# Kernel optimization log

Measured on AMD Instinct MI355X. Metric: run time of the kernel, lower is better.

## Reference

```python
import jax, jax.numpy as jnp
import numpy as np

DN = ('NCHW', 'OIHW', 'NCHW')

def conv2d(x, w, pad):
    return jax.lax.conv_general_dilated(x, w, (1, 1), [(pad, pad), (pad, pad)], dimension_numbers=DN)

def conv_module(x, w, g, b):
    # Conv2d -> BN (inference-mode per-channel affine) -> ReLU
    pad = (w.shape[-1] - 1) // 2
    y = conv2d(x, w, pad)
    return jax.nn.relu(y * g[None, :, None, None] + b[None, :, None, None])

def seq_conv_module(x, w, g, b):
    # x: (T, B, C, H, W) -> apply ConvModule per frame by folding T into batch
    T, B, C, H, W = x.shape
    y = conv_module(x.reshape(T * B, C, H, W), w, g, b)
    return y.reshape(T, B, -1, H, W)

def setup_inputs() -> dict:
    key = jax.random.key(0)
    ks = jax.random.split(key, 32)
    Cin, Ck, Cv, Cout = 1024, 256, 512, 512
    T, B, H, W = 4, 1, 64, 64
    s = 0.02
    d = {}
    d['x'] = jax.random.normal(ks[0], (B, Cin, H, W), jnp.float32)
    d['seq'] = jax.random.normal(ks[1], (T, B, Cin, H, W), jnp.float32)
    def mk_cm(i, cin, cout, k):
        return (jax.random.normal(ks[i], (cout, cin, k, k), jnp.float32) * s,
                jnp.ones((cout,), jnp.float32),
                jnp.zeros((cout,), jnp.float32))
    d['wk1'], d['gk1'], d['bk1'] = mk_cm(2, Cin, Ck, 1)
    d['wk2'], d['gk2'], d['bk2'] = mk_cm(3, Ck, Ck, 3)
    d['wv1'], d['gv1'], d['bv1'] = mk_cm(4, Cin, Cv, 1)
    d['wv2'], d['gv2'], d['bv2'] = mk_cm(5, Cv, Cv, 3)
    d['wqk1'], d['gqk1'], d['bqk1'] = mk_cm(6, Cin, Ck, 1)
    d['wqk2'], d['gqk2'], d['bqk2'] = mk_cm(7, Ck, Ck, 3)
    d['wqv1'], d['gqv1'], d['bqv1'] = mk_cm(8, Cin, Cv, 1)
    d['wqv2'], d['gqv2'], d['bqv2'] = mk_cm(9, Cv, Cv, 3)
    d['wb'], d['gb'], d['bb'] = mk_cm(10, 2 * Cv, Cout, 3)
    return d

def reference(x, seq, wk1, gk1, bk1, wk2, gk2, bk2, wv1, gv1, bv1, wv2, gv2, bv2,
              wqk1, gqk1, bqk1, wqk2, gqk2, bqk2, wqv1, gqv1, bqv1, wqv2, gqv2, bqv2,
              wb, gb, bb):
    # memory key/value convs over the T reference frames
    mk = seq_conv_module(seq_conv_module(seq, wk1, gk1, bk1), wk2, gk2, bk2)  # (T,B,Ck,H,W)
    mv = seq_conv_module(seq_conv_module(seq, wv1, gv1, bv1), wv2, gv2, bv2)  # (T,B,Cv,H,W)
    # query key/value convs on current frame
    qk = conv_module(conv_module(x, wqk1, gqk1, bqk1), wqk2, gqk2, bqk2)      # (B,Ck,H,W)
    qv = conv_module(conv_module(x, wqv1, gqv1, bqv1), wqv2, gqv2, bqv2)      # (B,Cv,H,W)
    T, B, Ck, H, W = mk.shape
    Cv = mv.shape[2]
    mk = jnp.transpose(mk, (1, 2, 0, 3, 4)).reshape(B, Ck, T * H * W)         # (B,Ck,THW)
    mv = jnp.transpose(mv, (1, 2, 0, 3, 4)).reshape(B, Cv, T * H * W)         # (B,Cv,THW)
    qkf = qk.reshape(B, Ck, H * W)                                            # (B,Ck,HW)
    # attention: (B,HW,THW); matmul_norm=False so no 1/sqrt(Ck) scaling
    attn = jax.nn.softmax(jnp.einsum('bcq,bck->bqk', qkf, mk), axis=-1)
    mem = jnp.einsum('bqk,bck->bcq', attn, mv).reshape(B, Cv, H, W)
    out = conv_module(jnp.concatenate([qv, mem], axis=1), wb, gb, bb)
    return out
```

## Files before the change

kernel.cpp:

```cpp
#include <hip/hip_runtime.h>
#include <stdint.h>


typedef short bf16x8 __attribute__((ext_vector_type(8)));
typedef float f32x4  __attribute__((ext_vector_type(4)));
typedef unsigned short u16x4 __attribute__((ext_vector_type(4)));

__device__ __forceinline__ unsigned short f2bf(float f) {
  union { float f; unsigned u; } x; x.f = f;
  unsigned r = x.u + 0x7FFFu + ((x.u >> 16) & 1u);
  return (unsigned short)(r >> 16);
}

typedef const __attribute__((address_space(1))) char* as1cp;
typedef __attribute__((address_space(3))) char* as3p;

__device__ __forceinline__ void gl_lds16(const char* g, char* l) {
  __builtin_amdgcn_global_load_lds((as1cp)g, (as3p)l, 16, 0, 0);
}

enum { EP_CL_BNR = 0, EP_CF_BNR_BF16 = 1, EP_CF_BNR_F32 = 2, EP_EXPSUM = 3,
       EP_PVDIV = 4, EP_PART = 5 };

template<int EP, bool CF, bool CONV3>
__global__ __launch_bounds__(256) void gemm_k(
    const unsigned short* __restrict__ Wp,
    const unsigned short* __restrict__ Xp,
    int K, int Kc, int Xstride, int Xcoloff, int cin_log2,
    void* __restrict__ Op, int Ostride, int Ocoloff, size_t plane,
    const float* __restrict__ g1, const float* __restrict__ b1,
    const float* __restrict__ g2, const float* __restrict__ b2, int gsplit,
    float* __restrict__ rowsum, const char* __restrict__ zp)
{
  __shared__ short Wt[2][128 * 32];
  __shared__ short Xt[2][128 * 32];
  const int tid = threadIdx.x;
  const int w = tid >> 6;
  const int l = tid & 63;
  const int m0 = blockIdx.y * 128;
  const int n0 = blockIdx.x * 128;
  const int wrow0 = CF ? n0 : m0;
  const int xrow0 = CF ? m0 : n0;

  const int ch0 = w, ch1 = w + 4;
  const int sr0 = ch0 * 16 + (l >> 2);
  const int sr1 = ch1 * 16 + (l >> 2);
  const int kbp = (l & 3) << 4;
  const int kbl0 = kbp ^ ((sr0 & 3) << 4);
  const int kbl1 = kbp ^ ((sr1 & 3) << 4);

  const size_t wrb = (size_t)K * 2;
  const size_t xrb = (size_t)Xstride * 2;

  const int wm = (w >> 1) * 64;
  const int wn = (w & 1) * 64;

  const int k_begin = blockIdx.z * Kc;
  const int k_end = (k_begin + Kc < K) ? (k_begin + Kc) : K;

  auto stage = [&](int b, int k0) {
    int ci0 = k0, kh = 1, kw = 1, dpos = 0;
    if (CONV3) {
      int e = k0 >> cin_log2;
      ci0 = k0 & ((1 << cin_log2) - 1);
      kh = e / 3; kw = e - kh * 3;
      dpos = (kh - 1) * 64 + (kw - 1);
    }
    char* Wl = (char*)&Wt[b][0];
    char* Xl = (char*)&Xt[b][0];
    gl_lds16((const char*)Wp + (size_t)(wrow0 + sr0) * wrb + (size_t)k0 * 2 + kbl0,
             Wl + ch0 * 1024);
    gl_lds16((const char*)Wp + (size_t)(wrow0 + sr1) * wrb + (size_t)k0 * 2 + kbl1,
             Wl + ch1 * 1024);
    const char* xs0;
    const char* xs1;
    if (CONV3) {
      int p = xrow0 + sr0;
      int hw = p & 4095;
      int h2 = (hw >> 6) + kh - 1, w2 = (hw & 63) + kw - 1;
      xs0 = ((unsigned)h2 < 64u && (unsigned)w2 < 64u)
          ? (const char*)Xp + (size_t)(p + dpos) * xrb + (size_t)(Xcoloff + ci0) * 2 + kbl0
          : zp + kbl0;
      p = xrow0 + sr1;
      hw = p & 4095;
      h2 = (hw >> 6) + kh - 1; w2 = (hw & 63) + kw - 1;
      xs1 = ((unsigned)h2 < 64u && (unsigned)w2 < 64u)
          ? (const char*)Xp + (size_t)(p + dpos) * xrb + (size_t)(Xcoloff + ci0) * 2 + kbl1
          : zp + kbl1;
    } else {
      xs0 = (const char*)Xp + (size_t)(xrow0 + sr0) * xrb + (size_t)(Xcoloff + k0) * 2 + kbl0;
      xs1 = (const char*)Xp + (size_t)(xrow0 + sr1) * xrb + (size_t)(Xcoloff + k0) * 2 + kbl1;
    }
    gl_lds16(xs0, Xl + ch0 * 1024);
    gl_lds16(xs1, Xl + ch1 * 1024);
  };

  f32x4 acc[4][4] = {};

  int cur = 0;
  stage(0, k_begin);
  for (int k0 = k_begin; k0 < k_end; k0 += 32) {
    if (k0 + 32 < k_end) {
      stage(cur ^ 1, k0 + 32);
      asm volatile("s_waitcnt vmcnt(4)" ::: "memory");
    } else {
      asm volatile("s_waitcnt vmcnt(0)" ::: "memory");
    }
    __builtin_amdgcn_s_barrier();

    const short* Wb = &Wt[cur][0];
    const short* Xb = &Xt[cur][0];
    const short* At = CF ? Xb : Wb;
    const short* Bt = CF ? Wb : Xb;

    bf16x8 af[4], bfv[4];
#pragma unroll
    for (int i = 0; i < 4; i++) {
      int row = wm + i * 16 + (l & 15);
      int kb = ((l >> 4) << 4) ^ ((row & 3) << 4);
      af[i] = *(const bf16x8*)(At + row * 32 + (kb >> 1));
    }
#pragma unroll
    for (int j = 0; j < 4; j++) {
      int row = wn + j * 16 + (l & 15);
      int kb = ((l >> 4) << 4) ^ ((row & 3) << 4);
      bfv[j] = *(const bf16x8*)(Bt + row * 32 + (kb >> 1));
    }
#pragma unroll
    for (int i = 0; i < 4; i++)
#pragma unroll
      for (int j = 0; j < 4; j++)
        acc[i][j] = __builtin_amdgcn_mfma_f32_16x16x32_bf16(af[i], bfv[j], acc[i][j], 0, 0, 0);

    __builtin_amdgcn_s_barrier();
    cur ^= 1;
  }

  const int col = l & 15;
  const int rb = (l >> 4) << 2;

  if constexpr (EP == EP_PART) {
    float* P = (float*)Op + (size_t)blockIdx.z * plane;
#pragma unroll
    for (int j = 0; j < 4; j++) {
      int gn = n0 + wn + j * 16 + col;
#pragma unroll
      for (int i = 0; i < 4; i++) {
        int gm = m0 + wm + i * 16 + rb;
        *(f32x4*)(P + (size_t)gn * Ostride + gm) = acc[i][j];
      }
    }
  }
  if constexpr (EP == EP_CL_BNR) {
#pragma unroll
    for (int i = 0; i < 4; i++) {
      int gm = m0 + wm + i * 16 + rb;
      const float* gp; const float* bp;
      if (gm < gsplit) { gp = g1 + gm; bp = b1 + gm; }
      else             { gp = g2 + (gm - gsplit); bp = b2 + (gm - gsplit); }
      float G[4], B[4];
#pragma unroll
      for (int r = 0; r < 4; r++) { G[r] = gp[r]; B[r] = bp[r]; }
#pragma unroll
      for (int j = 0; j < 4; j++) {
        int gn = n0 + wn + j * 16 + col;
        f32x4 v = acc[i][j];
        u16x4 o;
#pragma unroll
        for (int r = 0; r < 4; r++) o[r] = f2bf(fmaxf(v[r] * G[r] + B[r], 0.f));
        *(u16x4*)((unsigned short*)Op + (size_t)gn * Ostride + Ocoloff + gm) = o;
      }
    }
  }
  if constexpr (EP == EP_CF_BNR_BF16 || EP == EP_CF_BNR_F32) {
#pragma unroll
    for (int j = 0; j < 4; j++) {
      int gn = n0 + wn + j * 16 + col;
      float G = (gn < gsplit) ? g1[gn] : g2[gn - gsplit];
      float Bv = (gn < gsplit) ? b1[gn] : b2[gn - gsplit];
#pragma unroll
      for (int i = 0; i < 4; i++) {
        int gm = m0 + wm + i * 16 + rb;
        f32x4 v = acc[i][j];
        if constexpr (EP == EP_CF_BNR_F32) {
          f32x4 o;
#pragma unroll
          for (int r = 0; r < 4; r++) o[r] = fmaxf(v[r] * G + Bv, 0.f);
          *(f32x4*)((float*)Op + (size_t)gn * Ostride + Ocoloff + gm) = o;
        } else {
          u16x4 o;
#pragma unroll
          for (int r = 0; r < 4; r++) o[r] = f2bf(fmaxf(v[r] * G + Bv, 0.f));
          *(u16x4*)((unsigned short*)Op + (size_t)gn * Ostride + Ocoloff + gm) = o;
        }
      }
    }
  }
  if constexpr (EP == EP_EXPSUM) {
#pragma unroll
    for (int j = 0; j < 4; j++) {
      int gn = n0 + wn + j * 16 + col;
      float s = 0.f;
#pragma unroll
      for (int i = 0; i < 4; i++) {
        int gm = m0 + wm + i * 16 + rb;
        f32x4 v = acc[i][j];
        u16x4 o;
#pragma unroll
        for (int r = 0; r < 4; r++) { float e = __expf(v[r]); s += e; o[r] = f2bf(e); }
        *(u16x4*)((unsigned short*)Op + (size_t)gn * Ostride + gm) = o;
      }
      s += __shfl_xor(s, 16);
      s += __shfl_xor(s, 32);
      if (l < 16) atomicAdd(rowsum + gn, s);
    }
  }
  if constexpr (EP == EP_PVDIV) {
#pragma unroll
    for (int j = 0; j < 4; j++) {
      int gn = n0 + wn + j * 16 + col;
      float inv = 1.0f / rowsum[gn];
#pragma unroll
      for (int i = 0; i < 4; i++) {
        int gm = m0 + wm + i * 16 + rb;
        f32x4 v = acc[i][j];
        u16x4 o;
#pragma unroll
        for (int r = 0; r < 4; r++) o[r] = f2bf(v[r] * inv);
        *(u16x4*)((unsigned short*)Op + (size_t)gn * Ostride + Ocoloff + gm) = o;
      }
    }
  }
}

enum { RED_BNR_BF16 = 0, RED_PVDIV = 1, RED_BNR_F32 = 2 };

template<int MODE>
__global__ __launch_bounds__(256) void reduce_k(
    const float* __restrict__ P, int Z, size_t plane, int Cdim,
    void* __restrict__ out, int Ostride, int Ocoloff,
    const float* __restrict__ g1, const float* __restrict__ b1,
    const float* __restrict__ g2, const float* __restrict__ b2, int gsplit,
    const float* __restrict__ rowsum, int total4)
{
  int t = blockIdx.x * 256 + threadIdx.x;
  if (t >= total4) return;
  size_t base = (size_t)t * 4;
  int n = (int)(base / (size_t)Cdim);
  int c = (int)(base % (size_t)Cdim);
  f32x4 s = *(const f32x4*)(P + base);
  for (int z = 1; z < Z; z++) {
    f32x4 v = *(const f32x4*)(P + (size_t)z * plane + base);
    s += v;
  }
  if constexpr (MODE == RED_BNR_BF16) {
    u16x4 o;
#pragma unroll
    for (int r = 0; r < 4; r++) {
      int ch = c + r;
      float G = (ch < gsplit) ? g1[ch] : g2[ch - gsplit];
      float B = (ch < gsplit) ? b1[ch] : b2[ch - gsplit];
      o[r] = f2bf(fmaxf(s[r] * G + B, 0.f));
    }
    *(u16x4*)((unsigned short*)out + (size_t)n * Ostride + Ocoloff + c) = o;
  }
  if constexpr (MODE == RED_PVDIV) {
    float inv = 1.0f / rowsum[n];
    u16x4 o;
#pragma unroll
    for (int r = 0; r < 4; r++) o[r] = f2bf(s[r] * inv);
    *(u16x4*)((unsigned short*)out + (size_t)n * Ostride + Ocoloff + c) = o;
  }
  if constexpr (MODE == RED_BNR_F32) {
    float G = g1[n], B = b1[n];
    f32x4 o;
#pragma unroll
    for (int r = 0; r < 4; r++) o[r] = fmaxf(s[r] * G + B, 0.f);
    *(f32x4*)((float*)out + (size_t)n * Ostride + c) = o;
  }
}

__global__ __launch_bounds__(256) void nchw_to_cl(const float* __restrict__ src,
                                                  unsigned short* __restrict__ dst,
                                                  int C, int P) {
  __shared__ float t[32][33];
  int f = blockIdx.z;
  src += (size_t)f * C * P;
  dst += (size_t)f * C * P;
  int p0 = blockIdx.x * 32, c0 = blockIdx.y * 32;
  int a = threadIdx.x & 31, b = threadIdx.x >> 5;
#pragma unroll
  for (int k = 0; k < 4; k++)
    t[b + 8 * k][a] = src[(size_t)(c0 + b + 8 * k) * P + p0 + a];
  __syncthreads();
#pragma unroll
  for (int k = 0; k < 4; k++)
    dst[(size_t)(p0 + b + 8 * k) * C + c0 + a] = f2bf(t[a][b + 8 * k]);
}

__global__ __launch_bounds__(256) void cvt_bf16(const float* __restrict__ s,
                                                unsigned short* __restrict__ d, int n) {
  int i = blockIdx.x * 256 + threadIdx.x;
  if (i < n) d[i] = f2bf(s[i]);
}

__global__ __launch_bounds__(256) void repack3(const float* __restrict__ s,
                                               unsigned short* __restrict__ d,
                                               int ci_log2, int n) {
  int i = blockIdx.x * 256 + threadIdx.x;
  if (i >= n) return;
  int Ci = 1 << ci_log2;
  int ci = i & (Ci - 1);
  int t = i >> ci_log2;
  int e = t % 9;
  int co = t / 9;
  d[i] = f2bf(s[((size_t)co * Ci + ci) * 9 + e]);
}

__global__ __launch_bounds__(256) void fillf(float* p, float v, int n) {
  int i = blockIdx.x * 256 + threadIdx.x;
  if (i < n) p[i] = v;
}

extern "C" void kernel_launch(void* const* d_in, const int* in_sizes, int n_in,
                              void* d_out, int out_size, void* d_ws, size_t ws_size,
                              hipStream_t stream) {
  (void)in_sizes; (void)n_in;
  const float* x    = (const float*)d_in[0];
  const float* seq  = (const float*)d_in[1];
  const float* wk1  = (const float*)d_in[2];
  const float* gk1  = (const float*)d_in[3];
  const float* bk1  = (const float*)d_in[4];
  const float* wk2  = (const float*)d_in[5];
  const float* gk2  = (const float*)d_in[6];
  const float* bk2  = (const float*)d_in[7];
  const float* wv1  = (const float*)d_in[8];
  const float* gv1  = (const float*)d_in[9];
  const float* bv1  = (const float*)d_in[10];
  const float* wv2  = (const float*)d_in[11];
  const float* gv2  = (const float*)d_in[12];
  const float* bv2  = (const float*)d_in[13];
  const float* wqk1 = (const float*)d_in[14];
  const float* gqk1 = (const float*)d_in[15];
  const float* bqk1 = (const float*)d_in[16];
  const float* wqk2 = (const float*)d_in[17];
  const float* gqk2 = (const float*)d_in[18];
  const float* bqk2 = (const float*)d_in[19];
  const float* wqv1 = (const float*)d_in[20];
  const float* gqv1 = (const float*)d_in[21];
  const float* bqv1 = (const float*)d_in[22];
  const float* wqv2 = (const float*)d_in[23];
  const float* gqv2 = (const float*)d_in[24];
  const float* bqv2 = (const float*)d_in[25];
  const float* wb   = (const float*)d_in[26];
  const float* gb   = (const float*)d_in[27];
  const float* bb   = (const float*)d_in[28];

  char* ws = (char*)d_ws;
  size_t off = 0;
  auto alloc = [&](size_t bytes) { size_t o = off; off += (bytes + 255) & ~(size_t)255; return o; };
  size_t o_zp    = alloc(4096);
  size_t o_rs    = alloc(4096 * 4);
  size_t o_wKV1  = alloc((size_t)768 * 1024 * 2);
  size_t o_wQKV1 = alloc((size_t)768 * 1024 * 2);
  size_t o_wK2   = alloc((size_t)256 * 2304 * 2);
  size_t o_wQK2  = alloc((size_t)256 * 2304 * 2);
  size_t o_wV2   = alloc((size_t)512 * 4608 * 2);
  size_t o_wQV2  = alloc((size_t)512 * 4608 * 2);
  size_t o_wB    = alloc((size_t)512 * 9216 * 2);
  size_t o_mk    = alloc((size_t)16384 * 256 * 2);
  size_t o_mv    = alloc((size_t)512 * 16384 * 2);
  size_t o_qk    = alloc((size_t)4096 * 256 * 2);
  size_t o_qvm   = alloc((size_t)4096 * 1024 * 2);
  size_t o_part  = alloc((size_t)8 * 4096 * 512 * 4);
  size_t o_vol   = off;
  size_t o_xT    = o_vol;
  size_t o_seqT  = o_xT + (size_t)4096 * 1024 * 2;
  size_t o_kv1   = o_seqT + (size_t)4 * 4096 * 1024 * 2;
  size_t o_qkv1  = o_kv1 + (size_t)16384 * 768 * 2;
  size_t end1    = o_qkv1 + (size_t)4096 * 768 * 2;
  size_t o_expS  = o_vol;
  size_t end2    = o_expS + (size_t)4096 * 16384 * 2;
  size_t need    = end1 > end2 ? end1 : end2;

  bool SPLIT = ws_size >= need;
  if (!SPLIT) {
    size_t save = o_part;
    o_vol  = save;
    o_xT   = o_vol;
    o_seqT = o_xT + (size_t)4096 * 1024 * 2;
    o_kv1  = o_seqT + (size_t)4 * 4096 * 1024 * 2;
    o_qkv1 = o_kv1 + (size_t)16384 * 768 * 2;
    end1   = o_qkv1 + (size_t)4096 * 768 * 2;
    o_expS = o_vol;
    end2   = o_expS + (size_t)4096 * 16384 * 2;
    need   = end1 > end2 ? end1 : end2;
    if (ws_size < need) {
      fillf<<<(out_size + 255) / 256, 256, 0, stream>>>((float*)d_out, 12345.0f, out_size);
      return;
    }
  }

  const char* zp = ws + o_zp;
  float* rs = (float*)(ws + o_rs);
  unsigned short* wKV1p  = (unsigned short*)(ws + o_wKV1);
  unsigned short* wQKV1p = (unsigned short*)(ws + o_wQKV1);
  unsigned short* wK2p   = (unsigned short*)(ws + o_wK2);
  unsigned short* wQK2p  = (unsigned short*)(ws + o_wQK2);
  unsigned short* wV2p   = (unsigned short*)(ws + o_wV2);
  unsigned short* wQV2p  = (unsigned short*)(ws + o_wQV2);
  unsigned short* wBp    = (unsigned short*)(ws + o_wB);
  unsigned short* mkp    = (unsigned short*)(ws + o_mk);
  unsigned short* mvp    = (unsigned short*)(ws + o_mv);
  unsigned short* qkp    = (unsigned short*)(ws + o_qk);
  unsigned short* qvmp   = (unsigned short*)(ws + o_qvm);
  float* partp           = (float*)(ws + o_part);
  unsigned short* xTp    = (unsigned short*)(ws + o_xT);
  unsigned short* seqTp  = (unsigned short*)(ws + o_seqT);
  unsigned short* kv1p   = (unsigned short*)(ws + o_kv1);
  unsigned short* qkv1p  = (unsigned short*)(ws + o_qkv1);
  unsigned short* expSp  = (unsigned short*)(ws + o_expS);

  hipMemsetAsync(ws + o_zp, 0, 4096, stream);
  hipMemsetAsync(ws + o_rs, 0, 4096 * 4, stream);

  cvt_bf16<<<(256 * 1024 + 255) / 256, 256, 0, stream>>>(wk1, wKV1p, 256 * 1024);
  cvt_bf16<<<(512 * 1024 + 255) / 256, 256, 0, stream>>>(wv1, wKV1p + 256 * 1024, 512 * 1024);
  cvt_bf16<<<(256 * 1024 + 255) / 256, 256, 0, stream>>>(wqk1, wQKV1p, 256 * 1024);
  cvt_bf16<<<(512 * 1024 + 255) / 256, 256, 0, stream>>>(wqv1, wQKV1p + 256 * 1024, 512 * 1024);
  repack3<<<(256 * 2304 + 255) / 256, 256, 0, stream>>>(wk2, wK2p, 8, 256 * 2304);
  repack3<<<(256 * 2304 + 255) / 256, 256, 0, stream>>>(wqk2, wQK2p, 8, 256 * 2304);
  repack3<<<(512 * 4608 + 255) / 256, 256, 0, stream>>>(wv2, wV2p, 9, 512 * 4608);
  repack3<<<(512 * 4608 + 255) / 256, 256, 0, stream>>>(wqv2, wQV2p, 9, 512 * 4608);
  repack3<<<(512 * 9216 + 255) / 256, 256, 0, stream>>>(wb, wBp, 10, 512 * 9216);

  nchw_to_cl<<<dim3(128, 32, 1), 256, 0, stream>>>(x, xTp, 1024, 4096);
  nchw_to_cl<<<dim3(128, 32, 4), 256, 0, stream>>>(seq, seqTp, 1024, 4096);

  gemm_k<EP_CL_BNR, false, false><<<dim3(128, 6), 256, 0, stream>>>(
      wKV1p, seqTp, 1024, 1024, 1024, 0, 0, kv1p, 768, 0, 0,
      gk1, bk1, gv1, bv1, 256, rs, zp);
  if (SPLIT) {
    size_t plane = (size_t)4096 * 768;
    gemm_k<EP_PART, false, false><<<dim3(32, 6, 2), 256, 0, stream>>>(
        wQKV1p, xTp, 1024, 512, 1024, 0, 0, partp, 768, 0, plane,
        nullptr, nullptr, nullptr, nullptr, 0, rs, zp);
    int t4 = (int)(plane / 4);
    reduce_k<RED_BNR_BF16><<<(t4 + 255) / 256, 256, 0, stream>>>(
        partp, 2, plane, 768, qkv1p, 768, 0, gqk1, bqk1, gqv1, bqv1, 256, rs, t4);
  } else {
    gemm_k<EP_CL_BNR, false, false><<<dim3(32, 6), 256, 0, stream>>>(
        wQKV1p, xTp, 1024, 1024, 1024, 0, 0, qkv1p, 768, 0, 0,
        gqk1, bqk1, gqv1, bqv1, 256, rs, zp);
  }

  gemm_k<EP_CL_BNR, false, true><<<dim3(128, 2), 256, 0, stream>>>(
      wK2p, kv1p, 2304, 2304, 768, 0, 8, mkp, 256, 0, 0,
      gk2, bk2, gk2, bk2, 256, rs, zp);
  if (SPLIT) {
    size_t plane = (size_t)4096 * 256;
    gemm_k<EP_PART, false, true><<<dim3(32, 2, 4), 256, 0, stream>>>(
        wQK2p, qkv1p, 2304, 576, 768, 0, 8, partp, 256, 0, plane,
        nullptr, nullptr, nullptr, nullptr, 0, rs, zp);
    int t4 = (int)(plane / 4);
    reduce_k<RED_BNR_BF16><<<(t4 + 255) / 256, 256, 0, stream>>>(
        partp, 4, plane, 256, qkp, 256, 0, gqk2, bqk2, gqk2, bqk2, 256, rs, t4);
  } else {
    gemm_k<EP_CL_BNR, false, true><<<dim3(32, 2), 256, 0, stream>>>(
        wQK2p, qkv1p, 2304, 2304, 768, 0, 8, qkp, 256, 0, 0,
        gqk2, bqk2, gqk2, bqk2, 256, rs, zp);
  }
  if (SPLIT) {
    size_t plane = (size_t)4096 * 512;
    gemm_k<EP_PART, false, true><<<dim3(32, 4, 4), 256, 0, stream>>>(
        wQV2p, qkv1p, 4608, 1152, 768, 256, 9, partp, 512, 0, plane,
        nullptr, nullptr, nullptr, nullptr, 0, rs, zp);
    int t4 = (int)(plane / 4);
    reduce_k<RED_BNR_BF16><<<(t4 + 255) / 256, 256, 0, stream>>>(
        partp, 4, plane, 512, qvmp, 1024, 0, gqv2, bqv2, gqv2, bqv2, 512, rs, t4);
  } else {
    gemm_k<EP_CL_BNR, false, true><<<dim3(32, 4), 256, 0, stream>>>(
        wQV2p, qkv1p, 4608, 4608, 768, 256, 9, qvmp, 1024, 0, 0,
        gqv2, bqv2, gqv2, bqv2, 512, rs, zp);
  }
  gemm_k<EP_CF_BNR_BF16, true, true><<<dim3(4, 128), 256, 0, stream>>>(
      wV2p, kv1p, 4608, 4608, 768, 256, 9, mvp, 16384, 0, 0,
      gv2, bv2, gv2, bv2, 512, rs, zp);

  gemm_k<EP_EXPSUM, false, false><<<dim3(32, 128), 256, 0, stream>>>(
      mkp, qkp, 256, 256, 256, 0, 0, expSp, 16384, 0, 0,
      nullptr, nullptr, nullptr, nullptr, 1 << 30, rs, zp);
  if (SPLIT) {
    size_t plane = (size_t)4096 * 512;
    gemm_k<EP_PART, false, false><<<dim3(32, 4, 8), 256, 0, stream>>>(
        mvp, expSp, 16384, 2048, 16384, 0, 0, partp, 512, 0, plane,
        nullptr, nullptr, nullptr, nullptr, 0, rs, zp);
    int t4 = (int)(plane / 4);
    reduce_k<RED_PVDIV><<<(t4 + 255) / 256, 256, 0, stream>>>(
        partp, 8, plane, 512, qvmp, 1024, 512, nullptr, nullptr, nullptr, nullptr, 0, rs, t4);
  } else {
    gemm_k<EP_PVDIV, false, false><<<dim3(32, 4), 256, 0, stream>>>(
        mvp, expSp, 16384, 16384, 16384, 0, 0, qvmp, 1024, 512, 0,
        nullptr, nullptr, nullptr, nullptr, 1 << 30, rs, zp);
  }

  if (SPLIT) {
    size_t plane = (size_t)512 * 4096;
    gemm_k<EP_PART, true, true><<<dim3(4, 32, 4), 256, 0, stream>>>(
        wBp, qvmp, 9216, 2304, 1024, 0, 10, partp, 4096, 0, plane,
        nullptr, nullptr, nullptr, nullptr, 0, rs, zp);
    int t4 = (int)(plane / 4);
    reduce_k<RED_BNR_F32><<<(t4 + 255) / 256, 256, 0, stream>>>(
        partp, 4, plane, 4096, (float*)d_out, 4096, 0, gb, bb, gb, bb, 512, rs, t4);
  } else {
    gemm_k<EP_CF_BNR_F32, true, true><<<dim3(4, 32), 256, 0, stream>>>(
        wBp, qvmp, 9216, 9216, 1024, 0, 10, (float*)d_out, 4096, 0, 0,
        gb, bb, gb, bb, 512, rs, zp);
  }
}
```

Baseline: 646.3 us.

## Triple-buffer GEMM LDS pipeline and add wide-tile PV GEMM with blocked exp layout

Measured after the change: 627.3 us. -2.9%, faster.

```diff
diff --git a/kernel.cpp b/kernel.cpp
--- a/kernel.cpp
+++ b/kernel.cpp
@@ -32,8 +32,8 @@
     const float* __restrict__ g2, const float* __restrict__ b2, int gsplit,
     float* __restrict__ rowsum, const char* __restrict__ zp)
 {
-  __shared__ short Wt[2][128 * 32];
-  __shared__ short Xt[2][128 * 32];
+  __shared__ short Wt[3][128 * 32];
+  __shared__ short Xt[3][128 * 32];
   const int tid = threadIdx.x;
   const int w = tid >> 6;
   const int l = tid & 63;
@@ -57,6 +57,7 @@
 
   const int k_begin = blockIdx.z * Kc;
   const int k_end = (k_begin + Kc < K) ? (k_begin + Kc) : K;
+  const int niter = (k_end - k_begin) >> 5;
 
   auto stage = [&](int b, int k0) {
     int ci0 = k0, kh = 1, kw = 1, dpos = 0;
@@ -97,15 +98,16 @@
 
   f32x4 acc[4][4] = {};
 
+  {
+    int nst = niter < 3 ? niter : 3;
+    for (int s = 0; s < nst; ++s) stage(s, k_begin + (s << 5));
+  }
   int cur = 0;
-  stage(0, k_begin);
-  for (int k0 = k_begin; k0 < k_end; k0 += 32) {
-    if (k0 + 32 < k_end) {
-      stage(cur ^ 1, k0 + 32);
-      asm volatile("s_waitcnt vmcnt(4)" ::: "memory");
-    } else {
-      asm volatile("s_waitcnt vmcnt(0)" ::: "memory");
-    }
+  for (int i = 0; i < niter; ++i) {
+    int ahead = niter - i - 1;
+    if (ahead >= 2)      asm volatile("s_waitcnt vmcnt(8)" ::: "memory");
+    else if (ahead == 1) asm volatile("s_waitcnt vmcnt(4)" ::: "memory");
+    else                 asm volatile("s_waitcnt vmcnt(0)" ::: "memory");
     __builtin_amdgcn_s_barrier();
 
     const short* Wb = &Wt[cur][0];
@@ -115,10 +117,10 @@
 
     bf16x8 af[4], bfv[4];
 #pragma unroll
-    for (int i = 0; i < 4; i++) {
-      int row = wm + i * 16 + (l & 15);
+    for (int ii = 0; ii < 4; ii++) {
+      int row = wm + ii * 16 + (l & 15);
       int kb = ((l >> 4) << 4) ^ ((row & 3) << 4);
-      af[i] = *(const bf16x8*)(At + row * 32 + (kb >> 1));
+      af[ii] = *(const bf16x8*)(At + row * 32 + (kb >> 1));
     }
 #pragma unroll
     for (int j = 0; j < 4; j++) {
@@ -127,13 +129,14 @@
       bfv[j] = *(const bf16x8*)(Bt + row * 32 + (kb >> 1));
     }
 #pragma unroll
-    for (int i = 0; i < 4; i++)
+    for (int ii = 0; ii < 4; ii++)
 #pragma unroll
       for (int j = 0; j < 4; j++)
-        acc[i][j] = __builtin_amdgcn_mfma_f32_16x16x32_bf16(af[i], bfv[j], acc[i][j], 0, 0, 0);
+        acc[ii][j] = __builtin_amdgcn_mfma_f32_16x16x32_bf16(af[ii], bfv[j], acc[ii][j], 0, 0, 0);
 
     __builtin_amdgcn_s_barrier();
-    cur ^= 1;
+    if (i + 3 < niter) stage(cur, k_begin + ((i + 3) << 5));
+    cur = cur == 2 ? 0 : cur + 1;
   }
 
   const int col = l & 15;
@@ -208,7 +211,11 @@
         u16x4 o;
 #pragma unroll
         for (int r = 0; r < 4; r++) { float e = __expf(v[r]); s += e; o[r] = f2bf(e); }
-        *(u16x4*)((unsigned short*)Op + (size_t)gn * Ostride + gm) = o;
+        if (gsplit)
+          *(u16x4*)((unsigned short*)Op + (size_t)(gm >> 5) * ((size_t)Ostride * 32)
+                    + (size_t)gn * 32 + (gm & 31)) = o;
+        else
+          *(u16x4*)((unsigned short*)Op + (size_t)gn * Ostride + gm) = o;
       }
       s += __shfl_xor(s, 16);
       s += __shfl_xor(s, 32);
@@ -229,6 +236,98 @@
         for (int r = 0; r < 4; r++) o[r] = f2bf(v[r] * inv);
         *(u16x4*)((unsigned short*)Op + (size_t)gn * Ostride + Ocoloff + gm) = o;
       }
+    }
+  }
+}
+
+__global__ __launch_bounds__(512, 2) void pv_gemm(
+    const unsigned short* __restrict__ Wp,
+    const unsigned short* __restrict__ Xp,
+    int K, int Kc, int qtot,
+    float* __restrict__ P, size_t plane)
+{
+  __shared__ short Wt[3][512 * 32];
+  __shared__ short Xt[3][128 * 32];
+  const int tid = threadIdx.x;
+  const int w = tid >> 6;
+  const int l = tid & 63;
+  const int n0 = blockIdx.x * 128;
+  const int z = blockIdx.y;
+  const int k_begin = z * Kc;
+  const int niter = Kc >> 5;
+  const int kbp = (l & 3) << 4;
+  const size_t wrb = (size_t)K * 2;
+
+  auto stage = [&](int b, int k0) {
+    char* Wl = (char*)&Wt[b][0];
+    char* Xl = (char*)&Xt[b][0];
+#pragma unroll
+    for (int t = 0; t < 4; ++t) {
+      int sr = w * 64 + t * 16 + (l >> 2);
+      int c = kbp ^ ((sr & 3) << 4);
+      gl_lds16((const char*)Wp + (size_t)sr * wrb + (size_t)k0 * 2 + c,
+               Wl + (w * 4 + t) * 1024);
+    }
+    int sx = w * 16 + (l >> 2);
+    int cx = kbp ^ ((sx & 3) << 4);
+    gl_lds16((const char*)Xp + (size_t)(k0 >> 5) * ((size_t)qtot * 64)
+             + (size_t)(n0 + sx) * 64 + cx,
+             Xl + w * 1024);
+  };
+
+  const int wm = (w >> 1) * 128;
+  const int wn = (w & 1) * 64;
+
+  f32x4 acc[8][4] = {};
+
+  {
+    int nst = niter < 3 ? niter : 3;
+    for (int s = 0; s < nst; ++s) stage(s, k_begin + (s << 5));
+  }
+  int cur = 0;
+  for (int i = 0; i < niter; ++i) {
+    int ahead = niter - i - 1;
+    if (ahead >= 2)      asm volatile("s_waitcnt vmcnt(10)" ::: "memory");
+    else if (ahead == 1) asm volatile("s_waitcnt vmcnt(5)" ::: "memory");
+    else                 asm volatile("s_waitcnt vmcnt(0)" ::: "memory");
+    __builtin_amdgcn_s_barrier();
+
+    const short* Wb = &Wt[cur][0];
+    const short* Xb = &Xt[cur][0];
+    bf16x8 af[8], bfv[4];
+#pragma unroll
+    for (int ii = 0; ii < 8; ii++) {
+      int row = wm + ii * 16 + (l & 15);
+      int kb = ((l >> 4) << 4) ^ ((row & 3) << 4);
+      af[ii] = *(const bf16x8*)(Wb + row * 32 + (kb >> 1));
+    }
+#pragma unroll
+    for (int j = 0; j < 4; j++) {
+      int row = wn + j * 16 + (l & 15);
+      int kb = ((l >> 4) << 4) ^ ((row & 3) << 4);
+      bfv[j] = *(const bf16x8*)(Xb + row * 32 + (kb >> 1));
+    }
+#pragma unroll
+    for (int ii = 0; ii < 8; ii++)
+#pragma unroll
+      for (int j = 0; j < 4; j++)
+        acc[ii][j] = __builtin_amdgcn_mfma_f32_16x16x32_bf16(af[ii], bfv[j], acc[ii][j], 0, 0, 0);
+
+    __builtin_amdgcn_s_barrier();
+    if (i + 3 < niter) stage(cur, k_begin + ((i + 3) << 5));
+    cur = cur == 2 ? 0 : cur + 1;
+  }
+
+  float* Pz = P + (size_t)z * plane;
+  const int col = l & 15;
+  const int rb = (l >> 4) << 2;
+#pragma unroll
+  for (int j = 0; j < 4; j++) {
+    int gn = n0 + wn + j * 16 + col;
+#pragma unroll
+    for (int ii = 0; ii < 8; ii++) {
+      int gm = wm + ii * 16 + rb;
+      *(f32x4*)(Pz + (size_t)gn * 512 + gm) = acc[ii][j];
     }
   }
 }
@@ -487,21 +586,23 @@
       wV2p, kv1p, 4608, 4608, 768, 256, 9, mvp, 16384, 0, 0,
       gv2, bv2, gv2, bv2, 512, rs, zp);
 
-  gemm_k<EP_EXPSUM, false, false><<<dim3(32, 128), 256, 0, stream>>>(
-      mkp, qkp, 256, 256, 256, 0, 0, expSp, 16384, 0, 0,
-      nullptr, nullptr, nullptr, nullptr, 1 << 30, rs, zp);
   if (SPLIT) {
+    gemm_k<EP_EXPSUM, false, false><<<dim3(32, 128), 256, 0, stream>>>(
+        mkp, qkp, 256, 256, 256, 0, 0, expSp, 4096, 0, 0,
+        nullptr, nullptr, nullptr, nullptr, 1, rs, zp);
     size_t plane = (size_t)4096 * 512;
-    gemm_k<EP_PART, false, false><<<dim3(32, 4, 8), 256, 0, stream>>>(
-        mvp, expSp, 16384, 2048, 16384, 0, 0, partp, 512, 0, plane,
-        nullptr, nullptr, nullptr, nullptr, 0, rs, zp);
+    pv_gemm<<<dim3(32, 8), 512, 0, stream>>>(
+        mvp, expSp, 16384, 2048, 4096, partp, plane);
     int t4 = (int)(plane / 4);
     reduce_k<RED_PVDIV><<<(t4 + 255) / 256, 256, 0, stream>>>(
         partp, 8, plane, 512, qvmp, 1024, 512, nullptr, nullptr, nullptr, nullptr, 0, rs, t4);
   } else {
+    gemm_k<EP_EXPSUM, false, false><<<dim3(32, 128), 256, 0, stream>>>(
+        mkp, qkp, 256, 256, 256, 0, 0, expSp, 16384, 0, 0,
+        nullptr, nullptr, nullptr, nullptr, 0, rs, zp);
     gemm_k<EP_PVDIV, false, false><<<dim3(32, 4), 256, 0, stream>>>(
         mvp, expSp, 16384, 16384, 16384, 0, 0, qvmp, 1024, 512, 0,
-        nullptr, nullptr, nullptr, nullptr, 1 << 30, rs, zp);
+        nullptr, nullptr, nullptr, nullptr, 0, rs, zp);
   }
 
   if (SPLIT) {
```

## Store exp scores in k-slab tiled layout and deepen split-K across conv GEMMs

Applied to the files above, without the earlier changes.

After: 625.5 us. 3.2% less time.

```diff
diff --git a/kernel.cpp b/kernel.cpp
--- a/kernel.cpp
+++ b/kernel.cpp
@@ -22,7 +22,7 @@
 enum { EP_CL_BNR = 0, EP_CF_BNR_BF16 = 1, EP_CF_BNR_F32 = 2, EP_EXPSUM = 3,
        EP_PVDIV = 4, EP_PART = 5 };
 
-template<int EP, bool CF, bool CONV3>
+template<int EP, bool CF, bool CONV3, bool XTILED>
 __global__ __launch_bounds__(256) void gemm_k(
     const unsigned short* __restrict__ Wp,
     const unsigned short* __restrict__ Xp,
@@ -74,7 +74,11 @@
              Wl + ch1 * 1024);
     const char* xs0;
     const char* xs1;
-    if (CONV3) {
+    if constexpr (XTILED) {
+      size_t kslab = (size_t)(k0 >> 5) * ((size_t)Xstride * 64);
+      xs0 = (const char*)Xp + kslab + (size_t)(xrow0 + sr0) * 64 + kbl0;
+      xs1 = (const char*)Xp + kslab + (size_t)(xrow0 + sr1) * 64 + kbl1;
+    } else if constexpr (CONV3) {
       int p = xrow0 + sr0;
       int hw = p & 4095;
       int h2 = (hw >> 6) + kh - 1, w2 = (hw & 63) + kw - 1;
@@ -208,7 +212,11 @@
         u16x4 o;
 #pragma unroll
         for (int r = 0; r < 4; r++) { float e = __expf(v[r]); s += e; o[r] = f2bf(e); }
-        *(u16x4*)((unsigned short*)Op + (size_t)gn * Ostride + gm) = o;
+        if (gsplit)
+          *(u16x4*)((unsigned short*)Op + (size_t)(gm >> 5) * ((size_t)Ostride * 32)
+                    + (size_t)gn * 32 + (gm & 31)) = o;
+        else
+          *(u16x4*)((unsigned short*)Op + (size_t)gn * Ostride + gm) = o;
       }
       s += __shfl_xor(s, 16);
       s += __shfl_xor(s, 32);
@@ -233,7 +241,7 @@
   }
 }
 
-enum { RED_BNR_BF16 = 0, RED_PVDIV = 1, RED_BNR_F32 = 2 };
+enum { RED_BNR_BF16 = 0, RED_PVDIV = 1, RED_BNR_F32 = 2, RED_BNR_BF16_N = 3 };
 
 template<int MODE>
 __global__ __launch_bounds__(256) void reduce_k(
@@ -262,6 +270,13 @@
       float B = (ch < gsplit) ? b1[ch] : b2[ch - gsplit];
       o[r] = f2bf(fmaxf(s[r] * G + B, 0.f));
     }
+    *(u16x4*)((unsigned short*)out + (size_t)n * Ostride + Ocoloff + c) = o;
+  }
+  if constexpr (MODE == RED_BNR_BF16_N) {
+    float G = g1[n], B = b1[n];
+    u16x4 o;
+#pragma unroll
+    for (int r = 0; r < 4; r++) o[r] = f2bf(fmaxf(s[r] * G + B, 0.f));
     *(u16x4*)((unsigned short*)out + (size_t)n * Ostride + Ocoloff + c) = o;
   }
   if constexpr (MODE == RED_PVDIV) {
@@ -437,83 +452,100 @@
   nchw_to_cl<<<dim3(128, 32, 1), 256, 0, stream>>>(x, xTp, 1024, 4096);
   nchw_to_cl<<<dim3(128, 32, 4), 256, 0, stream>>>(seq, seqTp, 1024, 4096);
 
-  gemm_k<EP_CL_BNR, false, false><<<dim3(128, 6), 256, 0, stream>>>(
+  gemm_k<EP_CL_BNR, false, false, false><<<dim3(128, 6), 256, 0, stream>>>(
       wKV1p, seqTp, 1024, 1024, 1024, 0, 0, kv1p, 768, 0, 0,
       gk1, bk1, gv1, bv1, 256, rs, zp);
+
   if (SPLIT) {
-    size_t plane = (size_t)4096 * 768;
-    gemm_k<EP_PART, false, false><<<dim3(32, 6, 2), 256, 0, stream>>>(
-        wQKV1p, xTp, 1024, 512, 1024, 0, 0, partp, 768, 0, plane,
-        nullptr, nullptr, nullptr, nullptr, 0, rs, zp);
-    int t4 = (int)(plane / 4);
-    reduce_k<RED_BNR_BF16><<<(t4 + 255) / 256, 256, 0, stream>>>(
-        partp, 2, plane, 768, qkv1p, 768, 0, gqk1, bqk1, gqv1, bqv1, 256, rs, t4);
+    {
+      size_t plane = (size_t)4096 * 768;
+      gemm_k<EP_PART, false, false, false><<<dim3(32, 6, 4), 256, 0, stream>>>(
+          wQKV1p, xTp, 1024, 256, 1024, 0, 0, partp, 768, 0, plane,
+          nullptr, nullptr, nullptr, nullptr, 0, rs, zp);
+      int t4 = (int)(plane / 4);
+      reduce_k<RED_BNR_BF16><<<(t4 + 255) / 256, 256, 0, stream>>>(
+          partp, 4, plane, 768, qkv1p, 768, 0, gqk1, bqk1, gqv1, bqv1, 256, rs, t4);
+    }
+    {
+      size_t plane = (size_t)16384 * 256;
+      gemm_k<EP_PART, false, true, false><<<dim3(128, 2, 4), 256, 0, stream>>>(
+          wK2p, kv1p, 2304, 576, 768, 0, 8, partp, 256, 0, plane,
+          nullptr, nullptr, nullptr, nullptr, 0, rs, zp);
+      int t4 = (int)(plane / 4);
+      reduce_k<RED_BNR_BF16><<<(t4 + 255) / 256, 256, 0, stream>>>(
+          partp, 4, plane, 256, mkp, 256, 0, gk2, bk2, gk2, bk2, 256, rs, t4);
+    }
+    {
+      size_t plane = (size_t)4096 * 256;
+      gemm_k<EP_PART, false, true, false><<<dim3(32, 2, 8), 256, 0, stream>>>(
+          wQK2p, qkv1p, 2304, 288, 768, 0, 8, partp, 256, 0, plane,
+          nullptr, nullptr, nullptr, nullptr, 0, rs, zp);
+      int t4 = (int)(plane / 4);
+      reduce_k<RED_BNR_BF16><<<(t4 + 255) / 256, 256, 0, stream>>>(
+          partp, 8, plane, 256, qkp, 256, 0, gqk2, bqk2, gqk2, bqk2, 256, rs, t4);
+    }
+    {
+      size_t plane = (size_t)4096 * 512;
+      gemm_k<EP_PART, false, true, false><<<dim3(32, 4, 8), 256, 0, stream>>>(
+          wQV2p, qkv1p, 4608, 576, 768, 256, 9, partp, 512, 0, plane,
+          nullptr, nullptr, nullptr, nullptr, 0, rs, zp);
+      int t4 = (int)(plane / 4);
+      reduce_k<RED_BNR_BF16><<<(t4 + 255) / 256, 256, 0, stream>>>(
+          partp, 8, plane, 512, qvmp, 1024, 0, gqv2, bqv2, gqv2, bqv2, 512, rs, t4);
+    }
+    {
+      size_t plane = (size_t)512 * 16384;
+      gemm_k<EP_PART, true, true, false><<<dim3(4, 128, 2), 256, 0, stream>>>(
+          wV2p, kv1p, 4608, 2304, 768, 256, 9, partp, 16384, 0, plane,
+          nullptr, nullptr, nullptr, nullptr, 0, rs, zp);
+      int t4 = (int)(plane / 4);
+      reduce_k<RED_BNR_BF16_N><<<(t4 + 255) / 256, 256, 0, stream>>>(
+          partp, 2, plane, 16384, mvp, 16384, 0, gv2, bv2, nullptr, nullptr, 0, rs, t4);
+    }
+    gemm_k<EP_EXPSUM, false, false, false><<<dim3(32, 128), 256, 0, stream>>>(
+        mkp, qkp, 256, 256, 256, 0, 0, expSp, 4096, 0, 0,
+        nullptr, nullptr, nullptr, nullptr, 1, rs, zp);
+    {
+      size_t plane = (size_t)4096 * 512;
+      gemm_k<EP_PART, false, false, true><<<dim3(32, 4, 8), 256, 0, stream>>>(
+          mvp, expSp, 16384, 2048, 4096, 0, 0, partp, 512, 0, plane,
+          nullptr, nullptr, nullptr, nullptr, 0, rs, zp);
+      int t4 = (int)(plane / 4);
+      reduce_k<RED_PVDIV><<<(t4 + 255) / 256, 256, 0, stream>>>(
+          partp, 8, plane, 512, qvmp, 1024, 512, nullptr, nullptr, nullptr, nullptr, 0, rs, t4);
+    }
+    {
+      size_t plane = (size_t)512 * 4096;
+      gemm_k<EP_PART, true, true, false><<<dim3(4, 32, 8), 256, 0, stream>>>(
+          wBp, qvmp, 9216, 1152, 1024, 0, 10, partp, 4096, 0, plane,
+          nullptr, nullptr, nullptr, nullptr, 0, rs, zp);
+      int t4 = (int)(plane / 4);
+      reduce_k<RED_BNR_F32><<<(t4 + 255) / 256, 256, 0, stream>>>(
+          partp, 8, plane, 4096, (float*)d_out, 4096, 0, gb, bb, gb, bb, 512, rs, t4);
+    }
   } else {
-    gemm_k<EP_CL_BNR, false, false><<<dim3(32, 6), 256, 0, stream>>>(
+    gemm_k<EP_CL_BNR, false, false, false><<<dim3(32, 6), 256, 0, stream>>>(
         wQKV1p, xTp, 1024, 1024, 1024, 0, 0, qkv1p, 768, 0, 0,
         gqk1, bqk1, gqv1, bqv1, 256, rs, zp);
-  }
-
-  gemm_k<EP_CL_BNR, false, true><<<dim3(128, 2), 256, 0, stream>>>(
-      wK2p, kv1p, 2304, 2304, 768, 0, 8, mkp, 256, 0, 0,
-      gk2, bk2, gk2, bk2, 256, rs, zp);
-  if (SPLIT) {
-    size_t plane = (size_t)4096 * 256;
-    gemm_k<EP_PART, false, true><<<dim3(32, 2, 4), 256, 0, stream>>>(
-        wQK2p, qkv1p, 2304, 576, 768, 0, 8, partp, 256, 0, plane,
-        nullptr, nullptr, nullptr, nullptr, 0, rs, zp);
-    int t4 = (int)(plane / 4);
-    reduce_k<RED_BNR_BF16><<<(t4 + 255) / 256, 256, 0, stream>>>(
-        partp, 4, plane, 256, qkp, 256, 0, gqk2, bqk2, gqk2, bqk2, 256, rs, t4);
-  } else {
-    gemm_k<EP_CL_BNR, false, true><<<dim3(32, 2), 256, 0, stream>>>(
+    gemm_k<EP_CL_BNR, false, true, false><<<dim3(128, 2), 256, 0, stream>>>(
+        wK2p, kv1p, 2304, 2304, 768, 0, 8, mkp, 256, 0, 0,
+        gk2, bk2, gk2, bk2, 256, rs, zp);
+    gemm_k<EP_CL_BNR, false, true, false><<<dim3(32, 2), 256, 0, stream>>>(
         wQK2p, qkv1p, 2304, 2304, 768, 0, 8, qkp, 256, 0, 0,
         gqk2, bqk2, gqk2, bqk2, 256, rs, zp);
-  }
-  if (SPLIT) {
-    size_t plane = (size_t)4096 * 512;
-    gemm_k<EP_PART, false, true><<<dim3(32, 4, 4), 256, 0, stream>>>(
-        wQV2p, qkv1p, 4608, 1152, 768, 256, 9, partp, 512, 0, plane,
-        nullptr, nullptr, nullptr, nullptr, 0, rs, zp);
-    int t4 = (int)(plane / 4);
-    reduce_k<RED_BNR_BF16><<<(t4 + 255) / 256, 256, 0, stream>>>(
-        partp, 4, plane, 512, qvmp, 1024, 0, gqv2, bqv2, gqv2, bqv2, 512, rs, t4);
-  } else {
-    gemm_k<EP_CL_BNR, false, true><<<dim3(32, 4), 256, 0, stream>>>(
+    gemm_k<EP_CL_BNR, false, true, false><<<dim3(32, 4), 256, 0, stream>>>(
         wQV2p, qkv1p, 4608, 4608, 768, 256, 9, qvmp, 1024, 0, 0,
         gqv2, bqv2, gqv2, bqv2, 512, rs, zp);
-  }
-  gemm_k<EP_CF_BNR_BF16, true, true><<<dim3(4, 128), 256, 0, stream>>>(
-      wV2p, kv1p, 4608, 4608, 768, 256, 9, mvp, 16384, 0, 0,
-      gv2, bv2, gv2, bv2, 512, rs, zp);
-
-  gemm_k<EP_EXPSUM, false, false><<<dim3(32, 128), 256, 0, stream>>>(
-      mkp, qkp, 256, 256, 256, 0, 0, expSp, 16384, 0, 0,
-      nullptr, nullptr, nullptr, nullptr, 1 << 30, rs, zp);
-  if (SPLIT) {
-    size_t plane = (size_t)4096 * 512;
-    gemm_k<EP_PART, false, false><<<dim3(32, 4, 8), 256, 0, stream>>>(
-        mvp, expSp, 16384, 2048, 16384, 0, 0, partp, 512, 0, plane,
+    gemm_k<EP_CF_BNR_BF16, true, true, false><<<dim3(4, 128), 256, 0, stream>>>(
+        wV2p, kv1p, 4608, 4608, 768, 256, 9, mvp, 16384, 0, 0,
+        gv2, bv2, gv2, bv2, 512, rs, zp);
+    gemm_k<EP_EXPSUM, false, false, false><<<dim3(32, 128), 256, 0, stream>>>(
+        mkp, qkp, 256, 256, 256, 0, 0, expSp, 16384, 0, 0,
         nullptr, nullptr, nullptr, nullptr, 0, rs, zp);
-    int t4 = (int)(plane / 4);
-    reduce_k<RED_PVDIV><<<(t4 + 255) / 256, 256, 0, stream>>>(
-        partp, 8, plane, 512, qvmp, 1024, 512, nullptr, nullptr, nullptr, nullptr, 0, rs, t4);
-  } else {
-    gemm_k<EP_PVDIV, false, false><<<dim3(32, 4), 256, 0, stream>>>(
+    gemm_k<EP_PVDIV, false, false, false><<<dim3(32, 4), 256, 0, stream>>>(
         mvp, expSp, 16384, 16384, 16384, 0, 0, qvmp, 1024, 512, 0,
-        nullptr, nullptr, nullptr, nullptr, 1 << 30, rs, zp);
-  }
-
-  if (SPLIT) {
-    size_t plane = (size_t)512 * 4096;
-    gemm_k<EP_PART, true, true><<<dim3(4, 32, 4), 256, 0, stream>>>(
-        wBp, qvmp, 9216, 2304, 1024, 0, 10, partp, 4096, 0, plane,
         nullptr, nullptr, nullptr, nullptr, 0, rs, zp);
-    int t4 = (int)(plane / 4);
-    reduce_k<RED_BNR_F32><<<(t4 + 255) / 256, 256, 0, stream>>>(
-        partp, 4, plane, 4096, (float*)d_out, 4096, 0, gb, bb, gb, bb, 512, rs, t4);
-  } else {
-    gemm_k<EP_CF_BNR_F32, true, true><<<dim3(4, 32), 256, 0, stream>>>(
+    gemm_k<EP_CF_BNR_F32, true, true, false><<<dim3(4, 32), 256, 0, stream>>>(
         wBp, qvmp, 9216, 9216, 1024, 0, 10, (float*)d_out, 4096, 0, 0,
         gb, bb, gb, bb, 512, rs, zp);
   }
```
